# Optimization experiments

Measured on AMD Instinct MI355X. Metric: run time of the kernel, lower is better.

## Reference

```python
import jax, jax.numpy as jnp
import numpy as np

B, T, D, F, H, HID, OUT = 256, 512, 768, 1024, 8, 512, 256
EPS = 1e-5

def setup_inputs() -> dict:
    key = jax.random.key(0)
    ks = jax.random.split(key, 16)
    s = lambda fan_in: 1.0 / np.sqrt(fan_in)
    return {
        "x": jax.random.normal(ks[0], (B, F), jnp.float32),
        "text_feat": jax.random.normal(ks[1], (B, T, D), jnp.float32),
        "attention_mask": jax.random.randint(ks[2], (B, T), 0, 2, jnp.int32),
        # cross-attention params (torch Linear weight layout [out,in])
        "Wq": jax.random.normal(ks[3], (F, F), jnp.float32) * s(F),
        "bq": jnp.zeros((F,), jnp.float32),
        "Wk": jax.random.normal(ks[4], (F, D), jnp.float32) * s(D),
        "bk": jnp.zeros((F,), jnp.float32),
        "Wv": jax.random.normal(ks[5], (F, D), jnp.float32) * s(D),
        "bv": jnp.zeros((F,), jnp.float32),
        "Wo": jax.random.normal(ks[6], (F, F), jnp.float32) * s(F),
        "bo": jnp.zeros((F,), jnp.float32),
        # MLP: hidden Linear -> BatchNorm1d -> GELU, then output Linear
        "W1": jax.random.normal(ks[7], (HID, F), jnp.float32) * s(F),
        "b1": jnp.zeros((HID,), jnp.float32),
        "gamma": jnp.ones((HID,), jnp.float32),
        "beta": jnp.zeros((HID,), jnp.float32),
        "W2": jax.random.normal(ks[8], (OUT, HID), jnp.float32) * s(HID),
        "b2": jnp.zeros((OUT,), jnp.float32),
    }

def _forward(x, text_feat, attention_mask, Wq, bq, Wk, bk, Wv, bv, Wo, bo,
             W1, b1, gamma, beta, W2, b2):
    d = F // H
    q = (x @ Wq.T + bq).reshape(B, H, d)                      # [B,H,d] (q_len=1)
    k = (text_feat @ Wk.T + bk).reshape(B, T, H, d)           # [B,T,H,d]
    v = (text_feat @ Wv.T + bv).reshape(B, T, H, d)
    attn = jnp.einsum('bhd,bthd->bht', q, k) / jnp.sqrt(jnp.float32(d))
    attn = jnp.where(attention_mask[:, None, :] == 0, -jnp.inf, attn)
    attn = jax.nn.softmax(attn, axis=-1)                       # [B,H,T]
    out = jnp.einsum('bht,bthd->bhd', attn, v).reshape(B, F)
    out = out @ Wo.T + bo
    # MLP hidden: linear -> BatchNorm1d (training batch stats) -> GELU (exact)
    h = out @ W1.T + b1
    mu = jnp.mean(h, axis=0)
    var = jnp.var(h, axis=0)
    h = (h - mu) / jnp.sqrt(var + EPS) * gamma + beta
    h = jax.nn.gelu(h, approximate=False)
    return h @ W2.T + b2

def reference(x, text_feat, attention_mask, Wq, bq, Wk, bk, Wv, bv, Wo, bo,
              W1, b1, gamma, beta, W2, b2):
    return _forward(x, text_feat, attention_mask, Wq, bq, Wk, bk, Wv, bv, Wo, bo,
                    W1, b1, gamma, beta, W2, b2)
```

## Files before the change

kernel.cpp:

```cpp
#include <hip/hip_runtime.h>
#include <math.h>

#define Bb   256
#define Tt   512
#define Dd   768
#define Ff   1024
#define Hh   8
#define HIDh 512
#define OUTo 256

__device__ __forceinline__ void tr_tile4(const float* __restrict__ in,
                                         float* __restrict__ out,
                                         int R, int C, int cx, int ry,
                                         float (*tile)[33])
{
    int c0 = cx * 32, r0 = ry * 32;
    int r  = threadIdx.x >> 3;
    int c4 = (threadIdx.x & 7) * 4;
    float4 v = *(const float4*)&in[(size_t)(r0 + r) * C + c0 + c4];
    tile[r][c4 + 0] = v.x;
    tile[r][c4 + 1] = v.y;
    tile[r][c4 + 2] = v.z;
    tile[r][c4 + 3] = v.w;
    __syncthreads();
    float4 o;
    o.x = tile[c4 + 0][r];
    o.y = tile[c4 + 1][r];
    o.z = tile[c4 + 2][r];
    o.w = tile[c4 + 3][r];
    *(float4*)&out[(size_t)(c0 + r) * R + r0 + c4] = o;
}

__global__ __launch_bounds__(256) void prep(const float* __restrict__ Wq, float* __restrict__ WqT,
                                            const float* __restrict__ Wo, float* __restrict__ WoT,
                                            const float* __restrict__ Wv, float* __restrict__ WvT,
                                            const float* __restrict__ W1, float* __restrict__ W1T,
                                            const float* __restrict__ W2, float* __restrict__ W2T,
                                            const float* __restrict__ Wk, float* __restrict__ WkT)
{
    __shared__ float tile[32][33];
    int idx = blockIdx.x;
    if (idx < 1024) {
        tr_tile4(Wq, WqT, 1024, 1024, idx & 31, idx >> 5, tile);
    } else if (idx < 2048) {
        int i2 = idx - 1024;
        tr_tile4(Wo, WoT, 1024, 1024, i2 & 31, i2 >> 5, tile);
    } else if (idx < 2816) {
        int i2 = idx - 2048;
        tr_tile4(Wv, WvT, 1024, 768, i2 % 24, i2 / 24, tile);
    } else if (idx < 3328) {
        int i2 = idx - 2816;
        tr_tile4(W1, W1T, 512, 1024, i2 & 31, i2 >> 5, tile);
    } else if (idx < 3456) {
        int i2 = idx - 3328;
        tr_tile4(W2, W2T, 256, 512, i2 & 15, i2 >> 4, tile);
    } else {
        int i2 = idx - 3456;
        int i = i2 >> 3, h = i2 & 7;
        if (threadIdx.x < 192) {
            int j = threadIdx.x * 4;
            *(float4*)&WkT[(size_t)(i * 8 + h) * 768 + j] =
                *(const float4*)&Wk[(size_t)(h * 128 + i) * 768 + j];
        }
    }
}

#define FMA16(acc, a, w0, w1, w2, w3)                         \
    acc.x = fmaf(a.x, w0.x, acc.x); acc.y = fmaf(a.x, w0.y, acc.y); \
    acc.z = fmaf(a.x, w0.z, acc.z); acc.w = fmaf(a.x, w0.w, acc.w); \
    acc.x = fmaf(a.y, w1.x, acc.x); acc.y = fmaf(a.y, w1.y, acc.y); \
    acc.z = fmaf(a.y, w1.z, acc.z); acc.w = fmaf(a.y, w1.w, acc.w); \
    acc.x = fmaf(a.z, w2.x, acc.x); acc.y = fmaf(a.z, w2.y, acc.y); \
    acc.z = fmaf(a.z, w2.z, acc.z); acc.w = fmaf(a.z, w2.w, acc.w); \
    acc.x = fmaf(a.w, w3.x, acc.x); acc.y = fmaf(a.w, w3.y, acc.y); \
    acc.z = fmaf(a.w, w3.z, acc.z); acc.w = fmaf(a.w, w3.w, acc.w);

template<int CT, int RT, int R, int KS>
__global__ __launch_bounds__(256, 4) void gemm_sk(const float* __restrict__ A, int strideA,
                                                  const float* __restrict__ Wt, int N,
                                                  float* __restrict__ Cslab, int M)
{
    constexpr int CG = CT / 4;
    constexpr int RG = RT / R;
    static_assert(CG * RG == 256, "bad tile");
    const int cg = threadIdx.x % CG;
    const int rg = threadIdx.x / CG;
    const int n0 = blockIdx.x * CT + cg * 4;
    const int r0 = blockIdx.y * RT;
    const int k0 = blockIdx.z * KS;

    __shared__ float As[RT][KS + 4];
    for (int e = threadIdx.x * 4; e < RT * KS; e += 1024) {
        int r = e / KS, k = e % KS;
        *(float4*)&As[r][k] = *(const float4*)&A[(size_t)(r0 + r) * strideA + k0 + k];
    }
    __syncthreads();

    float4 acc[R];
#pragma unroll
    for (int rr = 0; rr < R; ++rr) acc[rr] = make_float4(0.f, 0.f, 0.f, 0.f);
    const float* wp = Wt + (size_t)k0 * N + n0;
#pragma unroll 2
    for (int k = 0; k < KS; k += 4) {
        float4 w0 = *(const float4*)&wp[(size_t)(k + 0) * N];
        float4 w1 = *(const float4*)&wp[(size_t)(k + 1) * N];
        float4 w2 = *(const float4*)&wp[(size_t)(k + 2) * N];
        float4 w3 = *(const float4*)&wp[(size_t)(k + 3) * N];
#pragma unroll
        for (int rr = 0; rr < R; ++rr) {
            float4 a = *(const float4*)&As[rg * R + rr][k];
            FMA16(acc[rr], a, w0, w1, w2, w3)
        }
    }
    float* cp = Cslab + (size_t)blockIdx.z * M * N;
#pragma unroll
    for (int rr = 0; rr < R; ++rr)
        *(float4*)&cp[(size_t)(r0 + rg * R + rr) * N + n0] = acc[rr];
}

template<int S>
__global__ __launch_bounds__(256) void reduce_add(const float* __restrict__ slabs,
                                                  size_t slabstride,
                                                  const float* __restrict__ bias,
                                                  float* __restrict__ out, int N, int total)
{
    int i4 = (blockIdx.x * 256 + threadIdx.x) * 4;
    if (i4 >= total) return;
    float4 acc = *(const float4*)&bias[i4 % N];
#pragma unroll
    for (int s = 0; s < S; ++s) {
        float4 v = *(const float4*)(slabs + (size_t)s * slabstride + i4);
        acc.x += v.x; acc.y += v.y; acc.z += v.z; acc.w += v.w;
    }
    *(float4*)&out[i4] = acc;
}

__global__ __launch_bounds__(256, 4) void qk_gemm(const float* __restrict__ qfull,
                                                  const float* __restrict__ WkT,
                                                  float* __restrict__ qkfull)
{
    const int cg = threadIdx.x & 15;
    const int rg = threadIdx.x >> 4;
    const int cb = blockIdx.x, rb = blockIdx.y;
    const int n0 = cb * 64 + cg * 4;
    const int r0 = rb * 64;
    const int aoff = ((cb * 64) / 768) * 128;

    __shared__ float As[64][132];
    for (int e = threadIdx.x * 4; e < 64 * 128; e += 1024) {
        int r = e >> 7, k = e & 127;
        *(float4*)&As[r][k] = *(const float4*)&qfull[(size_t)(r0 + r) * 1024 + aoff + k];
    }
    __syncthreads();

    float4 acc[4];
#pragma unroll
    for (int rr = 0; rr < 4; ++rr) acc[rr] = make_float4(0.f, 0.f, 0.f, 0.f);
    const float* wp = WkT + n0;
#pragma unroll 2
    for (int k = 0; k < 128; k += 4) {
        float4 w0 = *(const float4*)&wp[(size_t)(k + 0) * 6144];
        float4 w1 = *(const float4*)&wp[(size_t)(k + 1) * 6144];
        float4 w2 = *(const float4*)&wp[(size_t)(k + 2) * 6144];
        float4 w3 = *(const float4*)&wp[(size_t)(k + 3) * 6144];
#pragma unroll
        for (int rr = 0; rr < 4; ++rr) {
            float4 a = *(const float4*)&As[rg * 4 + rr][k];
            FMA16(acc[rr], a, w0, w1, w2, w3)
        }
    }
#pragma unroll
    for (int rr = 0; rr < 4; ++rr)
        *(float4*)&qkfull[(size_t)(r0 + rg * 4 + rr) * 6144 + n0] = acc[rr];
}

__device__ __forceinline__ float dot12(float4 a0, float4 a1, float4 a2,
                                       float4 x0, float4 x1, float4 x2)
{
    float acc;
    acc = a0.x * x0.x;
    acc = fmaf(a0.y, x0.y, acc);
    acc = fmaf(a0.z, x0.z, acc);
    acc = fmaf(a0.w, x0.w, acc);
    acc = fmaf(a1.x, x1.x, acc);
    acc = fmaf(a1.y, x1.y, acc);
    acc = fmaf(a1.z, x1.z, acc);
    acc = fmaf(a1.w, x1.w, acc);
    acc = fmaf(a2.x, x2.x, acc);
    acc = fmaf(a2.y, x2.y, acc);
    acc = fmaf(a2.z, x2.z, acc);
    acc = fmaf(a2.w, x2.w, acc);
    return acc;
}

__global__ __launch_bounds__(256, 2) void attn_part(const float* __restrict__ text,
                                                    const int* __restrict__ mask,
                                                    const float* __restrict__ qk,
                                                    float* __restrict__ pctx,
                                                    float* __restrict__ psum)
{
    const int bx   = blockIdx.x;
    const int b    = bx >> 2;
    const int qt   = bx & 3;
    const int tid  = threadIdx.x;
    const int wv   = tid >> 6;
    const int lane = tid & 63;

    __shared__ float qk_s[Hh][Dd];
    __shared__ float ctx_s[Hh][Dd];
    __shared__ float wsum_s[4][Hh];
    __shared__ int   list_s[128];
    __shared__ int   wcnt_s[2];

    const float* qkp = qk + (size_t)b * (Hh * Dd);
    float* qf = (float*)qk_s;
    float* cf = (float*)ctx_s;
    for (int e = tid * 4; e < Hh * Dd; e += 1024) {
        *(float4*)&qf[e] = *(const float4*)&qkp[e];
        *(float4*)&cf[e] = make_float4(0.f, 0.f, 0.f, 0.f);
    }

    int m = 0, pre = 0, t = 0;
    if (wv < 2) {
        t = qt * 128 + wv * 64 + lane;
        m = mask[(size_t)b * Tt + t];
        unsigned long long bal = __ballot(m != 0);
        pre = __popcll(bal & ((1ull << lane) - 1ull));
        if (lane == 0) wcnt_s[wv] = __popcll(bal);
    }
    __syncthreads();
    if (wv < 2 && m) {
        int base = wv ? wcnt_s[0] : 0;
        list_s[base + pre] = t;
    }
    __syncthreads();
    const int cnt = wcnt_s[0] + wcnt_s[1];

    float s[Hh] = {0.f, 0.f, 0.f, 0.f, 0.f, 0.f, 0.f, 0.f};
    float4 cr[Hh][3];
#pragma unroll
    for (int h = 0; h < Hh; ++h)
#pragma unroll
        for (int c = 0; c < 3; ++c) cr[h][c] = make_float4(0.f, 0.f, 0.f, 0.f);

    const float scale = 0.08838834764831845f;
    const float* tbase = text + (size_t)b * Tt * Dd;

    int e = wv;
    float4 xa0, xa1, xa2, xb0, xb1, xb2;
    xa0 = xa1 = xa2 = make_float4(0.f, 0.f, 0.f, 0.f);
    xb0 = xb1 = xb2 = xa0;
    if (e < cnt) {
        const float* tp = tbase + (size_t)list_s[e] * Dd + 4 * lane;
        xa0 = *(const float4*)(tp);
        xa1 = *(const float4*)(tp + 256);
        xa2 = *(const float4*)(tp + 512);
        int e1 = (e + 4 < cnt) ? e + 4 : cnt - 1;
        const float* tq = tbase + (size_t)list_s[e1] * Dd + 4 * lane;
        xb0 = *(const float4*)(tq);
        xb1 = *(const float4*)(tq + 256);
        xb2 = *(const float4*)(tq + 512);
    }
    while (e < cnt) {
        int ei = (e + 8 < cnt) ? e + 8 : cnt - 1;
        const float* tc = tbase + (size_t)list_s[ei] * Dd + 4 * lane;
        float4 xc0 = *(const float4*)(tc);
        float4 xc1 = *(const float4*)(tc + 256);
        float4 xc2 = *(const float4*)(tc + 512);

        float p[Hh];
#pragma unroll
        for (int h = 0; h < Hh; ++h) {
            const float* qh = &qk_s[h][4 * lane];
            float4 a0 = *(const float4*)(qh);
            float4 a1 = *(const float4*)(qh + 256);
            float4 a2 = *(const float4*)(qh + 512);
            p[h] = dot12(a0, a1, a2, xa0, xa1, xa2);
        }
#pragma unroll
        for (int h = 0; h < Hh; ++h) {
            float v = p[h];
            v += __shfl_xor(v, 1);
            v += __shfl_xor(v, 2);
            v += __shfl_xor(v, 4);
            v += __shfl_xor(v, 8);
            v += __shfl_xor(v, 16);
            v += __shfl_xor(v, 32);
            float w = __expf(v * scale);
            s[h] += w;
            cr[h][0].x = fmaf(w, xa0.x, cr[h][0].x);
            cr[h][0].y = fmaf(w, xa0.y, cr[h][0].y);
            cr[h][0].z = fmaf(w, xa0.z, cr[h][0].z);
            cr[h][0].w = fmaf(w, xa0.w, cr[h][0].w);
            cr[h][1].x = fmaf(w, xa1.x, cr[h][1].x);
            cr[h][1].y = fmaf(w, xa1.y, cr[h][1].y);
            cr[h][1].z = fmaf(w, xa1.z, cr[h][1].z);
            cr[h][1].w = fmaf(w, xa1.w, cr[h][1].w);
            cr[h][2].x = fmaf(w, xa2.x, cr[h][2].x);
            cr[h][2].y = fmaf(w, xa2.y, cr[h][2].y);
            cr[h][2].z = fmaf(w, xa2.z, cr[h][2].z);
            cr[h][2].w = fmaf(w, xa2.w, cr[h][2].w);
        }
        xa0 = xb0; xa1 = xb1; xa2 = xb2;
        xb0 = xc0; xb1 = xc1; xb2 = xc2;
        e += 4;
    }

    if (lane == 0) {
#pragma unroll
        for (int h = 0; h < Hh; ++h) wsum_s[wv][h] = s[h];
    }

    for (int w4 = 0; w4 < 4; ++w4) {
        __syncthreads();
        if (wv == w4) {
#pragma unroll
            for (int h = 0; h < Hh; ++h) {
                float* cp = &ctx_s[h][4 * lane];
#pragma unroll
                for (int c = 0; c < 3; ++c) {
                    float4 cur = *(float4*)(cp + c * 256);
                    cur.x += cr[h][c].x;
                    cur.y += cr[h][c].y;
                    cur.z += cr[h][c].z;
                    cur.w += cr[h][c].w;
                    *(float4*)(cp + c * 256) = cur;
                }
            }
        }
    }
    __syncthreads();

    if (tid < Hh) {
        float S = wsum_s[0][tid] + wsum_s[1][tid] + wsum_s[2][tid] + wsum_s[3][tid];
        psum[(size_t)bx * Hh + tid] = S;
    }
    float* outp = pctx + (size_t)bx * (Hh * Dd);
    for (int e2 = tid * 4; e2 < Hh * Dd; e2 += 1024)
        *(float4*)&outp[e2] = *(const float4*)&cf[e2];
}

__global__ __launch_bounds__(256, 4) void v_gemm(const float* __restrict__ pctx,
                                                 const float* __restrict__ psum,
                                                 const float* __restrict__ WvT,
                                                 float* __restrict__ aoslab)
{
    const int cg = threadIdx.x & 31;
    const int rg = threadIdx.x >> 5;
    const int h = blockIdx.x, rb = blockIdx.y, ks = blockIdx.z;
    const int n0 = h * 128 + cg * 4;
    const int r0 = rb * 32;
    const int k0 = ks * 128;

    __shared__ float As[32][132];
    __shared__ float sv[32];

    if (threadIdx.x < 32) {
        int row = r0 + threadIdx.x;
        float S = 0.f;
#pragma unroll
        for (int i = 0; i < 4; ++i) S += psum[(size_t)(row * 4 + i) * Hh + h];
        sv[threadIdx.x] = 1.0f / S;
    }
    __syncthreads();
    for (int e = threadIdx.x * 4; e < 32 * 128; e += 1024) {
        int r = e >> 7, k = e & 127;
        size_t col = (size_t)h * 768 + k0 + k;
        float4 acc = make_float4(0.f, 0.f, 0.f, 0.f);
#pragma unroll
        for (int i = 0; i < 4; ++i) {
            float4 v = *(const float4*)&pctx[((size_t)(r0 + r) * 4 + i) * 6144 + col];
            acc.x += v.x; acc.y += v.y; acc.z += v.z; acc.w += v.w;
        }
        float svv = sv[r];
        acc.x *= svv; acc.y *= svv; acc.z *= svv; acc.w *= svv;
        *(float4*)&As[r][k] = acc;
    }
    __syncthreads();

    float4 acc[4];
#pragma unroll
    for (int rr = 0; rr < 4; ++rr) acc[rr] = make_float4(0.f, 0.f, 0.f, 0.f);
    const float* wp = WvT + (size_t)k0 * 1024 + n0;
#pragma unroll 2
    for (int k = 0; k < 128; k += 4) {
        float4 w0 = *(const float4*)&wp[(size_t)(k + 0) * 1024];
        float4 w1 = *(const float4*)&wp[(size_t)(k + 1) * 1024];
        float4 w2 = *(const float4*)&wp[(size_t)(k + 2) * 1024];
        float4 w3 = *(const float4*)&wp[(size_t)(k + 3) * 1024];
#pragma unroll
        for (int rr = 0; rr < 4; ++rr) {
            float4 a = *(const float4*)&As[rg * 4 + rr][k];
            FMA16(acc[rr], a, w0, w1, w2, w3)
        }
    }
    float* cp = aoslab + (size_t)ks * 262144;
#pragma unroll
    for (int rr = 0; rr < 4; ++rr)
        *(float4*)&cp[(size_t)(r0 + rg * 4 + rr) * 1024 + n0] = acc[rr];
}

__global__ __launch_bounds__(256) void bn_stats2(const float* __restrict__ h1full,
                                                 const float* __restrict__ gamma,
                                                 const float* __restrict__ beta,
                                                 float* __restrict__ scl,
                                                 float* __restrict__ shf)
{
    int c8 = threadIdx.x & 7, rg = threadIdx.x >> 3;
    int c = blockIdx.x * 8 + c8;
    float sum = 0.f, sq = 0.f;
    for (int r = rg; r < Bb; r += 32) {
        float v = h1full[(size_t)r * HIDh + c];
        sum += v;
        sq = fmaf(v, v, sq);
    }
    __shared__ float ss[32][8], sq_[32][8];
    ss[rg][c8] = sum; sq_[rg][c8] = sq;
    for (int off = 16; off > 0; off >>= 1) {
        __syncthreads();
        if (rg < off) { ss[rg][c8] += ss[rg + off][c8]; sq_[rg][c8] += sq_[rg + off][c8]; }
    }
    __syncthreads();
    if (rg == 0) {
        float mu  = ss[0][c8] * (1.0f / Bb);
        float var = sq_[0][c8] * (1.0f / Bb) - mu * mu;
        float g   = gamma[c] * rsqrtf(var + 1e-5f);
        scl[c] = g;
        shf[c] = fmaf(-mu, g, beta[c]);
    }
}

__global__ __launch_bounds__(256, 4) void gelu2(const float* __restrict__ h1full,
                                                const float* __restrict__ scl,
                                                const float* __restrict__ shf,
                                                const float* __restrict__ W2T,
                                                const float* __restrict__ b2,
                                                float* __restrict__ out)
{
    const int cg = threadIdx.x & 15;
    const int rg = threadIdx.x >> 4;
    const int n0 = blockIdx.x * 64 + cg * 4;
    const int r0 = blockIdx.y * 16;

    __shared__ float As[16][132];
    float4 acc = make_float4(0.f, 0.f, 0.f, 0.f);

    for (int k0 = 0; k0 < HIDh; k0 += 128) {
        __syncthreads();
        for (int e = threadIdx.x * 4; e < 2048; e += 1024) {
            int r = e >> 7, k = e & 127;
            float4 v  = *(const float4*)&h1full[(size_t)(r0 + r) * HIDh + k0 + k];
            float4 sc = *(const float4*)&scl[k0 + k];
            float4 sh = *(const float4*)&shf[k0 + k];
            float4 z;
            z.x = fmaf(v.x, sc.x, sh.x);
            z.y = fmaf(v.y, sc.y, sh.y);
            z.z = fmaf(v.z, sc.z, sh.z);
            z.w = fmaf(v.w, sc.w, sh.w);
            z.x = 0.5f * z.x * (1.0f + erff(z.x * 0.70710678118654752f));
            z.y = 0.5f * z.y * (1.0f + erff(z.y * 0.70710678118654752f));
            z.z = 0.5f * z.z * (1.0f + erff(z.z * 0.70710678118654752f));
            z.w = 0.5f * z.w * (1.0f + erff(z.w * 0.70710678118654752f));
            *(float4*)&As[r][k] = z;
        }
        __syncthreads();
        const float* wp = W2T + (size_t)k0 * OUTo + n0;
#pragma unroll 2
        for (int k = 0; k < 128; k += 4) {
            float4 w0 = *(const float4*)&wp[(size_t)(k + 0) * OUTo];
            float4 w1 = *(const float4*)&wp[(size_t)(k + 1) * OUTo];
            float4 w2 = *(const float4*)&wp[(size_t)(k + 2) * OUTo];
            float4 w3 = *(const float4*)&wp[(size_t)(k + 3) * OUTo];
            float4 a = *(const float4*)&As[rg][k];
            FMA16(acc, a, w0, w1, w2, w3)
        }
    }

    float4 bvv = *(const float4*)&b2[n0];
    acc.x += bvv.x; acc.y += bvv.y; acc.z += bvv.z; acc.w += bvv.w;
    *(float4*)&out[(size_t)(r0 + rg) * OUTo + n0] = acc;
}

extern "C" void kernel_launch(void* const* d_in, const int* in_sizes, int n_in,
                              void* d_out, int out_size, void* d_ws, size_t ws_size,
                              hipStream_t stream)
{
    const float* x     = (const float*)d_in[0];
    const float* text  = (const float*)d_in[1];
    const int*   amask = (const int*)d_in[2];
    const float* Wq    = (const float*)d_in[3];
    const float* bq    = (const float*)d_in[4];
    const float* Wk    = (const float*)d_in[5];
    const float* Wv    = (const float*)d_in[7];
    const float* bv    = (const float*)d_in[8];
    const float* Wo    = (const float*)d_in[9];
    const float* bo    = (const float*)d_in[10];
    const float* W1    = (const float*)d_in[11];
    const float* b1    = (const float*)d_in[12];
    const float* gamma = (const float*)d_in[13];
    const float* beta  = (const float*)d_in[14];
    const float* W2    = (const float*)d_in[15];
    const float* b2    = (const float*)d_in[16];

    float* ws     = (float*)d_ws;
    float* WqT    = ws;
    float* WoT    = WqT    + 1048576;
    float* WkT    = WoT    + 1048576;
    float* WvT    = WkT    + 786432;
    float* W1T    = WvT    + 786432;
    float* W2T    = W1T    + 524288;
    float* qslab  = W2T    + 131072;
    float* qfull  = qslab  + 2097152;
    float* qkfull = qfull  + 262144;
    float* pctx   = qkfull + 1572864;
    float* psum   = pctx   + 6291456;
    float* aoslab = psum   + 8192;
    float* aofull = aoslab + 1572864;
    float* oslab  = aofull + 262144;
    float* ofull  = oslab  + 2097152;
    float* h1slab = ofull  + 262144;
    float* h1full = h1slab + 1048576;
    float* scl    = h1full + 131072;
    float* shf    = scl    + 512;

    prep<<<4480, 256, 0, stream>>>(Wq, WqT, Wo, WoT, Wv, WvT, W1, W1T, W2, W2T, Wk, WkT);

    gemm_sk<64, 64, 4, 128><<<dim3(16, 4, 8), 256, 0, stream>>>(x, 1024, WqT, 1024, qslab, 256);
    reduce_add<8><<<256, 256, 0, stream>>>(qslab, 262144, bq, qfull, 1024, 262144);

    qk_gemm<<<dim3(96, 4), 256, 0, stream>>>(qfull, WkT, qkfull);

    attn_part<<<1024, 256, 0, stream>>>(text, amask, qkfull, pctx, psum);

    v_gemm<<<dim3(8, 8, 6), 256, 0, stream>>>(pctx, psum, WvT, aoslab);
    reduce_add<6><<<256, 256, 0, stream>>>(aoslab, 262144, bv, aofull, 1024, 262144);

    gemm_sk<64, 64, 4, 128><<<dim3(16, 4, 8), 256, 0, stream>>>(aofull, 1024, WoT, 1024, oslab, 256);
    reduce_add<8><<<256, 256, 0, stream>>>(oslab, 262144, bo, ofull, 1024, 262144);

    gemm_sk<64, 64, 4, 128><<<dim3(8, 4, 8), 256, 0, stream>>>(ofull, 1024, W1T, 512, h1slab, 256);
    reduce_add<8><<<128, 256, 0, stream>>>(h1slab, 131072, b1, h1full, 512, 131072);

    bn_stats2<<<64, 256, 0, stream>>>(h1full, gamma, beta, scl, shf);

    gelu2<<<dim3(4, 16), 256, 0, stream>>>(h1full, scl, shf, W2T, b2, (float*)d_out);
}
```

Baseline: 202.9 us.

## Fuse all stages into one cooperative persistent kernel with grid syncs

Replaces the chain of separate kernel launches with a single cooperative persistent kernel of 256 blocks x 512 threads that runs each stage as a phase separated by grid.sync(). GEMM tiles are widened to 128 columns, the attention phase is restructured to a per-batch layout with a smaller ctx buffer in place of pctx/psum partials, and a per-kernel fallback path is kept. The aim is to remove launch gaps and tail effects between the many small stages. In exchange, grid-wide barriers add synchronisation cost and the fixed 256-block grid limits parallelism for the larger phases such as attention.

After: 273.3 us. +34.7%, slower.

```diff
diff --git a/kernel.cpp b/kernel.cpp
--- a/kernel.cpp
+++ b/kernel.cpp
@@ -1,68 +1,65 @@
 #include <hip/hip_runtime.h>
+#include <hip/hip_cooperative_groups.h>
 #include <math.h>
+
+namespace cg = cooperative_groups;
 
 #define Bb   256
 #define Tt   512
 #define Dd   768
-#define Ff   1024
 #define Hh   8
 #define HIDh 512
 #define OUTo 256
 
-__device__ __forceinline__ void tr_tile4(const float* __restrict__ in,
-                                         float* __restrict__ out,
-                                         int R, int C, int cx, int ry,
-                                         float (*tile)[33])
-{
-    int c0 = cx * 32, r0 = ry * 32;
-    int r  = threadIdx.x >> 3;
-    int c4 = (threadIdx.x & 7) * 4;
-    float4 v = *(const float4*)&in[(size_t)(r0 + r) * C + c0 + c4];
-    tile[r][c4 + 0] = v.x;
-    tile[r][c4 + 1] = v.y;
-    tile[r][c4 + 2] = v.z;
-    tile[r][c4 + 3] = v.w;
-    __syncthreads();
-    float4 o;
-    o.x = tile[c4 + 0][r];
-    o.y = tile[c4 + 1][r];
-    o.z = tile[c4 + 2][r];
-    o.w = tile[c4 + 3][r];
-    *(float4*)&out[(size_t)(c0 + r) * R + r0 + c4] = o;
-}
-
-__global__ __launch_bounds__(256) void prep(const float* __restrict__ Wq, float* __restrict__ WqT,
-                                            const float* __restrict__ Wo, float* __restrict__ WoT,
-                                            const float* __restrict__ Wv, float* __restrict__ WvT,
-                                            const float* __restrict__ W1, float* __restrict__ W1T,
-                                            const float* __restrict__ W2, float* __restrict__ W2T,
-                                            const float* __restrict__ Wk, float* __restrict__ WkT)
-{
-    __shared__ float tile[32][33];
-    int idx = blockIdx.x;
-    if (idx < 1024) {
-        tr_tile4(Wq, WqT, 1024, 1024, idx & 31, idx >> 5, tile);
-    } else if (idx < 2048) {
-        int i2 = idx - 1024;
-        tr_tile4(Wo, WoT, 1024, 1024, i2 & 31, i2 >> 5, tile);
-    } else if (idx < 2816) {
-        int i2 = idx - 2048;
-        tr_tile4(Wv, WvT, 1024, 768, i2 % 24, i2 / 24, tile);
-    } else if (idx < 3328) {
-        int i2 = idx - 2816;
-        tr_tile4(W1, W1T, 512, 1024, i2 & 31, i2 >> 5, tile);
-    } else if (idx < 3456) {
-        int i2 = idx - 3328;
-        tr_tile4(W2, W2T, 256, 512, i2 & 15, i2 >> 4, tile);
-    } else {
-        int i2 = idx - 3456;
-        int i = i2 >> 3, h = i2 & 7;
-        if (threadIdx.x < 192) {
-            int j = threadIdx.x * 4;
-            *(float4*)&WkT[(size_t)(i * 8 + h) * 768 + j] =
-                *(const float4*)&Wk[(size_t)(h * 128 + i) * 768 + j];
-        }
-    }
+#define NBLK 256
+#define NTHR 512
+
+union SMem {
+    float tile[2][32][33];
+    struct { float As[64][132]; } g;
+    struct { float qk[Hh][Dd]; float ctx[Hh][Dd];
+             float wsum[Hh][Hh]; float sinv[Hh];
+             int list[Tt]; int wcnt[Hh]; } a;
+    struct { float As[32][132]; } ge;
+    struct { float ss[64][8]; float sq[64][8]; } bn;
+};
+
+struct Params {
+    const float *x, *text;
+    const int   *amask;
+    const float *Wq, *bq, *Wk, *Wv, *bv, *Wo, *bo;
+    const float *W1, *b1, *gamma, *beta, *W2, *b2;
+    float *out, *ws;
+};
+
+struct WS {
+    float *WqT, *WoT, *WkT, *WvT, *W1T, *W2T;
+    float *qslab, *qfull, *qkfull, *ctx;
+    float *aoslab, *aofull, *oslab, *ofull, *h1slab, *h1full, *scl, *shf;
+};
+
+__device__ __host__ inline WS make_ws(float* w)
+{
+    WS s;
+    s.WqT    = w;
+    s.WoT    = s.WqT    + 1048576;
+    s.WkT    = s.WoT    + 1048576;
+    s.WvT    = s.WkT    + 786432;
+    s.W1T    = s.WvT    + 786432;
+    s.W2T    = s.W1T    + 524288;
+    s.qslab  = s.W2T    + 131072;
+    s.qfull  = s.qslab  + 2097152;
+    s.qkfull = s.qfull  + 262144;
+    s.ctx    = s.qkfull + 1572864;
+    s.aoslab = s.ctx    + 1572864;
+    s.aofull = s.aoslab + 1572864;
+    s.oslab  = s.aofull + 262144;
+    s.ofull  = s.oslab  + 2097152;
+    s.h1slab = s.ofull  + 262144;
+    s.h1full = s.h1slab + 1048576;
+    s.scl    = s.h1full + 131072;
+    s.shf    = s.scl    + 512;
+    return s;
 }
 
 #define FMA16(acc, a, w0, w1, w2, w3)                         \
@@ -75,103 +72,145 @@
     acc.x = fmaf(a.w, w3.x, acc.x); acc.y = fmaf(a.w, w3.y, acc.y); \
     acc.z = fmaf(a.w, w3.z, acc.z); acc.w = fmaf(a.w, w3.w, acc.w);
 
-template<int CT, int RT, int R, int KS>
-__global__ __launch_bounds__(256, 4) void gemm_sk(const float* __restrict__ A, int strideA,
-                                                  const float* __restrict__ Wt, int N,
-                                                  float* __restrict__ Cslab, int M)
-{
-    constexpr int CG = CT / 4;
-    constexpr int RG = RT / R;
-    static_assert(CG * RG == 256, "bad tile");
-    const int cg = threadIdx.x % CG;
-    const int rg = threadIdx.x / CG;
-    const int n0 = blockIdx.x * CT + cg * 4;
-    const int r0 = blockIdx.y * RT;
-    const int k0 = blockIdx.z * KS;
-
-    __shared__ float As[RT][KS + 4];
-    for (int e = threadIdx.x * 4; e < RT * KS; e += 1024) {
-        int r = e / KS, k = e % KS;
+__device__ void ph_prep(SMem* sm, const Params& p, const WS& w, int nblk, int bid)
+{
+    const int half = threadIdx.x >> 8;
+    const int tid  = threadIdx.x & 255;
+    for (int base = bid * 2; base < 3456; base += nblk * 2) {
+        int idx = base + half;
+        const float* in; float* out; int R, C, cx, ry;
+        if (idx < 1024)      { in = p.Wq; out = w.WqT; R = 1024; C = 1024; cx = idx & 31; ry = idx >> 5; }
+        else if (idx < 2048) { int i2 = idx - 1024; in = p.Wo; out = w.WoT; R = 1024; C = 1024; cx = i2 & 31; ry = i2 >> 5; }
+        else if (idx < 2816) { int i2 = idx - 2048; in = p.Wv; out = w.WvT; R = 1024; C = 768;  cx = i2 % 24; ry = i2 / 24; }
+        else if (idx < 3328) { int i2 = idx - 2816; in = p.W1; out = w.W1T; R = 512;  C = 1024; cx = i2 & 31; ry = i2 >> 5; }
+        else                 { int i2 = idx - 3328; in = p.W2; out = w.W2T; R = 256;  C = 512;  cx = i2 & 15; ry = i2 >> 4; }
+        float (*tile)[33] = sm->tile[half];
+        int c0 = cx * 32, r0 = ry * 32;
+        int r = tid >> 3, c4 = (tid & 7) * 4;
+        float4 v = *(const float4*)&in[(size_t)(r0 + r) * C + c0 + c4];
+        tile[r][c4 + 0] = v.x;
+        tile[r][c4 + 1] = v.y;
+        tile[r][c4 + 2] = v.z;
+        tile[r][c4 + 3] = v.w;
+        __syncthreads();
+        float4 o;
+        o.x = tile[c4 + 0][r];
+        o.y = tile[c4 + 1][r];
+        o.z = tile[c4 + 2][r];
+        o.w = tile[c4 + 3][r];
+        *(float4*)&out[(size_t)(c0 + r) * R + r0 + c4] = o;
+        __syncthreads();
+    }
+    const float4* src = (const float4*)p.Wk;
+    float4* dst = (float4*)w.WkT;
+    for (int f = bid * NTHR + threadIdx.x; f < 196608; f += nblk * NTHR) {
+        int rem = f / 192, j4 = f % 192;
+        int i = rem >> 3, h = rem & 7;
+        dst[f] = src[(size_t)(h * 128 + i) * 192 + j4];
+    }
+}
+
+__device__ void gemm128x64(SMem* sm, const float* __restrict__ A, int strideA,
+                           const float* __restrict__ Wt, int N,
+                           float* __restrict__ Cslab, int cb, int rb, int ks)
+{
+    float (*As)[132] = sm->g.As;
+    const int cgi = threadIdx.x & 31;
+    const int rg  = threadIdx.x >> 5;
+    const int n0 = cb * 128 + cgi * 4;
+    const int r0 = rb * 64;
+    const int k0 = ks * 128;
+
+    for (int e = threadIdx.x * 4; e < 8192; e += 2048) {
+        int r = e >> 7, k = e & 127;
         *(float4*)&As[r][k] = *(const float4*)&A[(size_t)(r0 + r) * strideA + k0 + k];
     }
     __syncthreads();
 
-    float4 acc[R];
-#pragma unroll
-    for (int rr = 0; rr < R; ++rr) acc[rr] = make_float4(0.f, 0.f, 0.f, 0.f);
+    float4 acc[4];
+#pragma unroll
+    for (int rr = 0; rr < 4; ++rr) acc[rr] = make_float4(0.f, 0.f, 0.f, 0.f);
     const float* wp = Wt + (size_t)k0 * N + n0;
 #pragma unroll 2
-    for (int k = 0; k < KS; k += 4) {
+    for (int k = 0; k < 128; k += 4) {
         float4 w0 = *(const float4*)&wp[(size_t)(k + 0) * N];
         float4 w1 = *(const float4*)&wp[(size_t)(k + 1) * N];
         float4 w2 = *(const float4*)&wp[(size_t)(k + 2) * N];
         float4 w3 = *(const float4*)&wp[(size_t)(k + 3) * N];
 #pragma unroll
-        for (int rr = 0; rr < R; ++rr) {
-            float4 a = *(const float4*)&As[rg * R + rr][k];
-            FMA16(acc[rr], a, w0, w1, w2, w3)
-        }
-    }
-    float* cp = Cslab + (size_t)blockIdx.z * M * N;
-#pragma unroll
-    for (int rr = 0; rr < R; ++rr)
-        *(float4*)&cp[(size_t)(r0 + rg * R + rr) * N + n0] = acc[rr];
-}
-
-template<int S>
-__global__ __launch_bounds__(256) void reduce_add(const float* __restrict__ slabs,
-                                                  size_t slabstride,
-                                                  const float* __restrict__ bias,
-                                                  float* __restrict__ out, int N, int total)
-{
-    int i4 = (blockIdx.x * 256 + threadIdx.x) * 4;
-    if (i4 >= total) return;
-    float4 acc = *(const float4*)&bias[i4 % N];
-#pragma unroll
-    for (int s = 0; s < S; ++s) {
-        float4 v = *(const float4*)(slabs + (size_t)s * slabstride + i4);
-        acc.x += v.x; acc.y += v.y; acc.z += v.z; acc.w += v.w;
-    }
-    *(float4*)&out[i4] = acc;
-}
-
-__global__ __launch_bounds__(256, 4) void qk_gemm(const float* __restrict__ qfull,
-                                                  const float* __restrict__ WkT,
-                                                  float* __restrict__ qkfull)
-{
-    const int cg = threadIdx.x & 15;
-    const int rg = threadIdx.x >> 4;
-    const int cb = blockIdx.x, rb = blockIdx.y;
-    const int n0 = cb * 64 + cg * 4;
-    const int r0 = rb * 64;
-    const int aoff = ((cb * 64) / 768) * 128;
-
-    __shared__ float As[64][132];
-    for (int e = threadIdx.x * 4; e < 64 * 128; e += 1024) {
-        int r = e >> 7, k = e & 127;
-        *(float4*)&As[r][k] = *(const float4*)&qfull[(size_t)(r0 + r) * 1024 + aoff + k];
-    }
-    __syncthreads();
-
-    float4 acc[4];
-#pragma unroll
-    for (int rr = 0; rr < 4; ++rr) acc[rr] = make_float4(0.f, 0.f, 0.f, 0.f);
-    const float* wp = WkT + n0;
-#pragma unroll 2
-    for (int k = 0; k < 128; k += 4) {
-        float4 w0 = *(const float4*)&wp[(size_t)(k + 0) * 6144];
-        float4 w1 = *(const float4*)&wp[(size_t)(k + 1) * 6144];
-        float4 w2 = *(const float4*)&wp[(size_t)(k + 2) * 6144];
-        float4 w3 = *(const float4*)&wp[(size_t)(k + 3) * 6144];
-#pragma unroll
         for (int rr = 0; rr < 4; ++rr) {
             float4 a = *(const float4*)&As[rg * 4 + rr][k];
             FMA16(acc[rr], a, w0, w1, w2, w3)
         }
     }
+    float* cp = Cslab + (size_t)ks * Bb * N;
 #pragma unroll
     for (int rr = 0; rr < 4; ++rr)
-        *(float4*)&qkfull[(size_t)(r0 + rg * 4 + rr) * 6144 + n0] = acc[rr];
+        *(float4*)&cp[(size_t)(r0 + rg * 4 + rr) * N + n0] = acc[rr];
+}
+
+__device__ void ph_qgemm(SMem* sm, const Params& p, const WS& w, int nblk, int bid)
+{
+    for (int j = bid; j < 256; j += nblk) {
+        gemm128x64(sm, p.x, 1024, w.WqT, 1024, w.qslab, j & 7, (j >> 3) & 3, j >> 5);
+        __syncthreads();
+    }
+}
+
+__device__ void ph_ogemm(SMem* sm, const Params& p, const WS& w, int nblk, int bid)
+{
+    for (int j = bid; j < 256; j += nblk) {
+        gemm128x64(sm, w.aofull, 1024, w.WoT, 1024, w.oslab, j & 7, (j >> 3) & 3, j >> 5);
+        __syncthreads();
+    }
+}
+
+__device__ void ph_h1gemm(SMem* sm, const Params& p, const WS& w, int nblk, int bid)
+{
+    for (int j = bid; j < 128; j += nblk) {
+        gemm128x64(sm, w.ofull, 1024, w.W1T, 512, w.h1slab, j & 3, (j >> 2) & 3, j >> 4);
+        __syncthreads();
+    }
+}
+
+__device__ void ph_qk(SMem* sm, const Params& p, const WS& w, int nblk, int bid)
+{
+    for (int j = bid; j < 192; j += nblk) {
+        int cb = j % 48, rb = j / 48;
+        float (*As)[132] = sm->g.As;
+        const int cgi = threadIdx.x & 31;
+        const int rg  = threadIdx.x >> 5;
+        const int n0 = cb * 128 + cgi * 4;
+        const int r0 = rb * 64;
+        const int aoff = (cb / 6) * 128;
+
+        for (int e = threadIdx.x * 4; e < 8192; e += 2048) {
+            int r = e >> 7, k = e & 127;
+            *(float4*)&As[r][k] = *(const float4*)&w.qfull[(size_t)(r0 + r) * 1024 + aoff + k];
+        }
+        __syncthreads();
+
+        float4 acc[4];
+#pragma unroll
+        for (int rr = 0; rr < 4; ++rr) acc[rr] = make_float4(0.f, 0.f, 0.f, 0.f);
+        const float* wp = w.WkT + n0;
+#pragma unroll 2
+        for (int k = 0; k < 128; k += 4) {
+            float4 w0 = *(const float4*)&wp[(size_t)(k + 0) * 6144];
+            float4 w1 = *(const float4*)&wp[(size_t)(k + 1) * 6144];
+            float4 w2 = *(const float4*)&wp[(size_t)(k + 2) * 6144];
+            float4 w3 = *(const float4*)&wp[(size_t)(k + 3) * 6144];
+#pragma unroll
+            for (int rr = 0; rr < 4; ++rr) {
+                float4 a = *(const float4*)&As[rg * 4 + rr][k];
+                FMA16(acc[rr], a, w0, w1, w2, w3)
+            }
+        }
+#pragma unroll
+        for (int rr = 0; rr < 4; ++rr)
+            *(float4*)&w.qkfull[(size_t)(r0 + rg * 4 + rr) * 6144 + n0] = acc[rr];
+        __syncthreads();
+    }
 }
 
 __device__ __forceinline__ float dot12(float4 a0, float4 a1, float4 a2,
@@ -193,355 +232,376 @@
     return acc;
 }
 
-__global__ __launch_bounds__(256, 2) void attn_part(const float* __restrict__ text,
-                                                    const int* __restrict__ mask,
-                                                    const float* __restrict__ qk,
-                                                    float* __restrict__ pctx,
-                                                    float* __restrict__ psum)
-{
-    const int bx   = blockIdx.x;
-    const int b    = bx >> 2;
-    const int qt   = bx & 3;
-    const int tid  = threadIdx.x;
-    const int wv   = tid >> 6;
-    const int lane = tid & 63;
-
-    __shared__ float qk_s[Hh][Dd];
-    __shared__ float ctx_s[Hh][Dd];
-    __shared__ float wsum_s[4][Hh];
-    __shared__ int   list_s[128];
-    __shared__ int   wcnt_s[2];
-
-    const float* qkp = qk + (size_t)b * (Hh * Dd);
-    float* qf = (float*)qk_s;
-    float* cf = (float*)ctx_s;
-    for (int e = tid * 4; e < Hh * Dd; e += 1024) {
-        *(float4*)&qf[e] = *(const float4*)&qkp[e];
-        *(float4*)&cf[e] = make_float4(0.f, 0.f, 0.f, 0.f);
-    }
-
-    int m = 0, pre = 0, t = 0;
-    if (wv < 2) {
-        t = qt * 128 + wv * 64 + lane;
-        m = mask[(size_t)b * Tt + t];
-        unsigned long long bal = __ballot(m != 0);
-        pre = __popcll(bal & ((1ull << lane) - 1ull));
-        if (lane == 0) wcnt_s[wv] = __popcll(bal);
-    }
-    __syncthreads();
-    if (wv < 2 && m) {
-        int base = wv ? wcnt_s[0] : 0;
-        list_s[base + pre] = t;
-    }
-    __syncthreads();
-    const int cnt = wcnt_s[0] + wcnt_s[1];
-
-    float s[Hh] = {0.f, 0.f, 0.f, 0.f, 0.f, 0.f, 0.f, 0.f};
-    float4 cr[Hh][3];
-#pragma unroll
-    for (int h = 0; h < Hh; ++h)
-#pragma unroll
-        for (int c = 0; c < 3; ++c) cr[h][c] = make_float4(0.f, 0.f, 0.f, 0.f);
-
-    const float scale = 0.08838834764831845f;
-    const float* tbase = text + (size_t)b * Tt * Dd;
-
-    int e = wv;
-    float4 xa0, xa1, xa2, xb0, xb1, xb2;
-    xa0 = xa1 = xa2 = make_float4(0.f, 0.f, 0.f, 0.f);
-    xb0 = xb1 = xb2 = xa0;
-    if (e < cnt) {
-        const float* tp = tbase + (size_t)list_s[e] * Dd + 4 * lane;
-        xa0 = *(const float4*)(tp);
-        xa1 = *(const float4*)(tp + 256);
-        xa2 = *(const float4*)(tp + 512);
-        int e1 = (e + 4 < cnt) ? e + 4 : cnt - 1;
-        const float* tq = tbase + (size_t)list_s[e1] * Dd + 4 * lane;
-        xb0 = *(const float4*)(tq);
-        xb1 = *(const float4*)(tq + 256);
-        xb2 = *(const float4*)(tq + 512);
-    }
-    while (e < cnt) {
-        int ei = (e + 8 < cnt) ? e + 8 : cnt - 1;
-        const float* tc = tbase + (size_t)list_s[ei] * Dd + 4 * lane;
-        float4 xc0 = *(const float4*)(tc);
-        float4 xc1 = *(const float4*)(tc + 256);
-        float4 xc2 = *(const float4*)(tc + 512);
-
-        float p[Hh];
-#pragma unroll
-        for (int h = 0; h < Hh; ++h) {
-            const float* qh = &qk_s[h][4 * lane];
-            float4 a0 = *(const float4*)(qh);
-            float4 a1 = *(const float4*)(qh + 256);
-            float4 a2 = *(const float4*)(qh + 512);
-            p[h] = dot12(a0, a1, a2, xa0, xa1, xa2);
-        }
-#pragma unroll
-        for (int h = 0; h < Hh; ++h) {
-            float v = p[h];
-            v += __shfl_xor(v, 1);
-            v += __shfl_xor(v, 2);
-            v += __shfl_xor(v, 4);
-            v += __shfl_xor(v, 8);
-            v += __shfl_xor(v, 16);
-            v += __shfl_xor(v, 32);
-            float w = __expf(v * scale);
-            s[h] += w;
-            cr[h][0].x = fmaf(w, xa0.x, cr[h][0].x);
-            cr[h][0].y = fmaf(w, xa0.y, cr[h][0].y);
-            cr[h][0].z = fmaf(w, xa0.z, cr[h][0].z);
-            cr[h][0].w = fmaf(w, xa0.w, cr[h][0].w);
-            cr[h][1].x = fmaf(w, xa1.x, cr[h][1].x);
-            cr[h][1].y = fmaf(w, xa1.y, cr[h][1].y);
-            cr[h][1].z = fmaf(w, xa1.z, cr[h][1].z);
-            cr[h][1].w = fmaf(w, xa1.w, cr[h][1].w);
-            cr[h][2].x = fmaf(w, xa2.x, cr[h][2].x);
-            cr[h][2].y = fmaf(w, xa2.y, cr[h][2].y);
-            cr[h][2].z = fmaf(w, xa2.z, cr[h][2].z);
-            cr[h][2].w = fmaf(w, xa2.w, cr[h][2].w);
-        }
-        xa0 = xb0; xa1 = xb1; xa2 = xb2;
-        xb0 = xc0; xb1 = xc1; xb2 = xc2;
-        e += 4;
-    }
-
-    if (lane == 0) {
-#pragma unroll
-        for (int h = 0; h < Hh; ++h) wsum_s[wv][h] = s[h];
-    }
-
-    for (int w4 = 0; w4 < 4; ++w4) {
-        __syncthreads();
-        if (wv == w4) {
+__device__ void ph_attn(SMem* sm, const Params& p, const WS& w, int nblk, int bid)
+{
+    for (int b = bid; b < Bb; b += nblk) {
+        const int tid  = threadIdx.x;
+        const int wv   = tid >> 6;
+        const int lane = tid & 63;
+
+        float (*qk_s)[Dd]  = sm->a.qk;
+        float (*ctx_s)[Dd] = sm->a.ctx;
+        float (*wsum_s)[Hh] = sm->a.wsum;
+        int* list_s = sm->a.list;
+        int* wcnt_s = sm->a.wcnt;
+
+        const float* qkp = w.qkfull + (size_t)b * (Hh * Dd);
+        float* qf = (float*)qk_s;
+        float* cf = (float*)ctx_s;
+        for (int e = tid * 4; e < Hh * Dd; e += 2048) {
+            *(float4*)&qf[e] = *(const float4*)&qkp[e];
+            *(float4*)&cf[e] = make_float4(0.f, 0.f, 0.f, 0.f);
+        }
+
+        {
+            int m = p.amask[(size_t)b * Tt + tid];
+            unsigned long long bal = __ballot(m != 0);
+            int pre = __popcll(bal & ((1ull << lane) - 1ull));
+            if (lane == 0) wcnt_s[wv] = __popcll(bal);
+            __syncthreads();
+            if (m) {
+                int base = 0;
+                for (int v = 0; v < wv; ++v) base += wcnt_s[v];
+                list_s[base + pre] = tid;
+            }
+            __syncthreads();
+        }
+        int cnt = 0;
+#pragma unroll
+        for (int v = 0; v < Hh; ++v) cnt += wcnt_s[v];
+
+        float s[Hh] = {0.f, 0.f, 0.f, 0.f, 0.f, 0.f, 0.f, 0.f};
+        float4 cr[Hh][3];
+#pragma unroll
+        for (int h = 0; h < Hh; ++h)
+#pragma unroll
+            for (int c = 0; c < 3; ++c) cr[h][c] = make_float4(0.f, 0.f, 0.f, 0.f);
+
+        const float scale = 0.08838834764831845f;
+        const float* tbase = p.text + (size_t)b * Tt * Dd;
+
+        int e = wv;
+        float4 xa0, xa1, xa2, xb0, xb1, xb2;
+        xa0 = xa1 = xa2 = make_float4(0.f, 0.f, 0.f, 0.f);
+        xb0 = xb1 = xb2 = xa0;
+        if (e < cnt) {
+            const float* tp = tbase + (size_t)list_s[e] * Dd + 4 * lane;
+            xa0 = *(const float4*)(tp);
+            xa1 = *(const float4*)(tp + 256);
+            xa2 = *(const float4*)(tp + 512);
+            int e1 = (e + 8 < cnt) ? e + 8 : cnt - 1;
+            const float* tq = tbase + (size_t)list_s[e1] * Dd + 4 * lane;
+            xb0 = *(const float4*)(tq);
+            xb1 = *(const float4*)(tq + 256);
+            xb2 = *(const float4*)(tq + 512);
+        }
+        while (e < cnt) {
+            int ei = (e + 16 < cnt) ? e + 16 : cnt - 1;
+            const float* tc = tbase + (size_t)list_s[ei] * Dd + 4 * lane;
+            float4 xc0 = *(const float4*)(tc);
+            float4 xc1 = *(const float4*)(tc + 256);
+            float4 xc2 = *(const float4*)(tc + 512);
+
+            float pr[Hh];
 #pragma unroll
             for (int h = 0; h < Hh; ++h) {
-                float* cp = &ctx_s[h][4 * lane];
-#pragma unroll
-                for (int c = 0; c < 3; ++c) {
-                    float4 cur = *(float4*)(cp + c * 256);
-                    cur.x += cr[h][c].x;
-                    cur.y += cr[h][c].y;
-                    cur.z += cr[h][c].z;
-                    cur.w += cr[h][c].w;
-                    *(float4*)(cp + c * 256) = cur;
-                }
-            }
-        }
-    }
-    __syncthreads();
-
-    if (tid < Hh) {
-        float S = wsum_s[0][tid] + wsum_s[1][tid] + wsum_s[2][tid] + wsum_s[3][tid];
-        psum[(size_t)bx * Hh + tid] = S;
-    }
-    float* outp = pctx + (size_t)bx * (Hh * Dd);
-    for (int e2 = tid * 4; e2 < Hh * Dd; e2 += 1024)
-        *(float4*)&outp[e2] = *(const float4*)&cf[e2];
-}
-
-__global__ __launch_bounds__(256, 4) void v_gemm(const float* __restrict__ pctx,
-                                                 const float* __restrict__ psum,
-                                                 const float* __restrict__ WvT,
-                                                 float* __restrict__ aoslab)
-{
-    const int cg = threadIdx.x & 31;
-    const int rg = threadIdx.x >> 5;
-    const int h = blockIdx.x, rb = blockIdx.y, ks = blockIdx.z;
-    const int n0 = h * 128 + cg * 4;
-    const int r0 = rb * 32;
-    const int k0 = ks * 128;
-
-    __shared__ float As[32][132];
-    __shared__ float sv[32];
-
-    if (threadIdx.x < 32) {
-        int row = r0 + threadIdx.x;
-        float S = 0.f;
-#pragma unroll
-        for (int i = 0; i < 4; ++i) S += psum[(size_t)(row * 4 + i) * Hh + h];
-        sv[threadIdx.x] = 1.0f / S;
-    }
-    __syncthreads();
-    for (int e = threadIdx.x * 4; e < 32 * 128; e += 1024) {
-        int r = e >> 7, k = e & 127;
-        size_t col = (size_t)h * 768 + k0 + k;
-        float4 acc = make_float4(0.f, 0.f, 0.f, 0.f);
-#pragma unroll
-        for (int i = 0; i < 4; ++i) {
-            float4 v = *(const float4*)&pctx[((size_t)(r0 + r) * 4 + i) * 6144 + col];
-            acc.x += v.x; acc.y += v.y; acc.z += v.z; acc.w += v.w;
-        }
-        float svv = sv[r];
-        acc.x *= svv; acc.y *= svv; acc.z *= svv; acc.w *= svv;
-        *(float4*)&As[r][k] = acc;
-    }
-    __syncthreads();
-
-    float4 acc[4];
-#pragma unroll
-    for (int rr = 0; rr < 4; ++rr) acc[rr] = make_float4(0.f, 0.f, 0.f, 0.f);
-    const float* wp = WvT + (size_t)k0 * 1024 + n0;
-#pragma unroll 2
-    for (int k = 0; k < 128; k += 4) {
-        float4 w0 = *(const float4*)&wp[(size_t)(k + 0) * 1024];
-        float4 w1 = *(const float4*)&wp[(size_t)(k + 1) * 1024];
-        float4 w2 = *(const float4*)&wp[(size_t)(k + 2) * 1024];
-        float4 w3 = *(const float4*)&wp[(size_t)(k + 3) * 1024];
-#pragma unroll
-        for (int rr = 0; rr < 4; ++rr) {
-            float4 a = *(const float4*)&As[rg * 4 + rr][k];
-            FMA16(acc[rr], a, w0, w1, w2, w3)
-        }
-    }
-    float* cp = aoslab + (size_t)ks * 262144;
-#pragma unroll
-    for (int rr = 0; rr < 4; ++rr)
-        *(float4*)&cp[(size_t)(r0 + rg * 4 + rr) * 1024 + n0] = acc[rr];
-}
-
-__global__ __launch_bounds__(256) void bn_stats2(const float* __restrict__ h1full,
-                                                 const float* __restrict__ gamma,
-                                                 const float* __restrict__ beta,
-                                                 float* __restrict__ scl,
-                                                 float* __restrict__ shf)
-{
-    int c8 = threadIdx.x & 7, rg = threadIdx.x >> 3;
-    int c = blockIdx.x * 8 + c8;
-    float sum = 0.f, sq = 0.f;
-    for (int r = rg; r < Bb; r += 32) {
-        float v = h1full[(size_t)r * HIDh + c];
-        sum += v;
-        sq = fmaf(v, v, sq);
-    }
-    __shared__ float ss[32][8], sq_[32][8];
-    ss[rg][c8] = sum; sq_[rg][c8] = sq;
-    for (int off = 16; off > 0; off >>= 1) {
-        __syncthreads();
-        if (rg < off) { ss[rg][c8] += ss[rg + off][c8]; sq_[rg][c8] += sq_[rg + off][c8]; }
-    }
-    __syncthreads();
-    if (rg == 0) {
-        float mu  = ss[0][c8] * (1.0f / Bb);
-        float var = sq_[0][c8] * (1.0f / Bb) - mu * mu;
-        float g   = gamma[c] * rsqrtf(var + 1e-5f);
-        scl[c] = g;
-        shf[c] = fmaf(-mu, g, beta[c]);
-    }
-}
-
-__global__ __launch_bounds__(256, 4) void gelu2(const float* __restrict__ h1full,
-                                                const float* __restrict__ scl,
-                                                const float* __restrict__ shf,
-                                                const float* __restrict__ W2T,
-                                                const float* __restrict__ b2,
-                                                float* __restrict__ out)
-{
-    const int cg = threadIdx.x & 15;
-    const int rg = threadIdx.x >> 4;
-    const int n0 = blockIdx.x * 64 + cg * 4;
-    const int r0 = blockIdx.y * 16;
-
-    __shared__ float As[16][132];
-    float4 acc = make_float4(0.f, 0.f, 0.f, 0.f);
-
-    for (int k0 = 0; k0 < HIDh; k0 += 128) {
-        __syncthreads();
-        for (int e = threadIdx.x * 4; e < 2048; e += 1024) {
+                const float* qh = &qk_s[h][4 * lane];
+                float4 a0 = *(const float4*)(qh);
+                float4 a1 = *(const float4*)(qh + 256);
+                float4 a2 = *(const float4*)(qh + 512);
+                pr[h] = dot12(a0, a1, a2, xa0, xa1, xa2);
+            }
+#pragma unroll
+            for (int h = 0; h < Hh; ++h) {
+                float v = pr[h];
+                v += __shfl_xor(v, 1);
+                v += __shfl_xor(v, 2);
+                v += __shfl_xor(v, 4);
+                v += __shfl_xor(v, 8);
+                v += __shfl_xor(v, 16);
+                v += __shfl_xor(v, 32);
+                float wt = __expf(v * scale);
+                s[h] += wt;
+                cr[h][0].x = fmaf(wt, xa0.x, cr[h][0].x);
+                cr[h][0].y = fmaf(wt, xa0.y, cr[h][0].y);
+                cr[h][0].z = fmaf(wt, xa0.z, cr[h][0].z);
+                cr[h][0].w = fmaf(wt, xa0.w, cr[h][0].w);
+                cr[h][1].x = fmaf(wt, xa1.x, cr[h][1].x);
+                cr[h][1].y = fmaf(wt, xa1.y, cr[h][1].y);
+                cr[h][1].z = fmaf(wt, xa1.z, cr[h][1].z);
+                cr[h][1].w = fmaf(wt, xa1.w, cr[h][1].w);
+                cr[h][2].x = fmaf(wt, xa2.x, cr[h][2].x);
+                cr[h][2].y = fmaf(wt, xa2.y, cr[h][2].y);
+                cr[h][2].z = fmaf(wt, xa2.z, cr[h][2].z);
+                cr[h][2].w = fmaf(wt, xa2.w, cr[h][2].w);
+            }
+            xa0 = xb0; xa1 = xb1; xa2 = xb2;
+            xb0 = xc0; xb1 = xc1; xb2 = xc2;
+            e += 8;
+        }
+
+        if (lane == 0) {
+#pragma unroll
+            for (int h = 0; h < Hh; ++h) wsum_s[wv][h] = s[h];
+        }
+
+        for (int rnd = 0; rnd < 8; ++rnd) {
+            __syncthreads();
+            int h = (wv + rnd) & 7;
+            float* cp = &ctx_s[h][4 * lane];
+#pragma unroll
+            for (int c = 0; c < 3; ++c) {
+                float4 cu = *(float4*)(cp + c * 256);
+                cu.x += cr[h][c].x;
+                cu.y += cr[h][c].y;
+                cu.z += cr[h][c].z;
+                cu.w += cr[h][c].w;
+                *(float4*)(cp + c * 256) = cu;
+            }
+        }
+        __syncthreads();
+
+        if (tid < Hh) {
+            float S = 0.f;
+#pragma unroll
+            for (int v = 0; v < Hh; ++v) S += wsum_s[v][tid];
+            sm->a.sinv[tid] = 1.0f / S;
+        }
+        __syncthreads();
+
+        float* outp = w.ctx + (size_t)b * (Hh * Dd);
+        for (int e2 = tid * 4; e2 < Hh * Dd; e2 += 2048) {
+            float4 v = *(const float4*)&cf[e2];
+            float si = sm->a.sinv[e2 / Dd];
+            v.x *= si; v.y *= si; v.z *= si; v.w *= si;
+            *(float4*)&outp[e2] = v;
+        }
+        __syncthreads();
+    }
+}
+
+__device__ void ph_v(SMem* sm, const Params& p, const WS& w, int nblk, int bid)
+{
+    for (int j = bid; j < 192; j += nblk) {
+        int h = j & 7, rb = (j >> 3) & 3, ks = j >> 5;
+        float (*As)[132] = sm->g.As;
+        const int cgi = threadIdx.x & 31;
+        const int rg  = threadIdx.x >> 5;
+        const int n0 = h * 128 + cgi * 4;
+        const int r0 = rb * 64;
+        const int k0 = ks * 128;
+
+        for (int e = threadIdx.x * 4; e < 8192; e += 2048) {
             int r = e >> 7, k = e & 127;
-            float4 v  = *(const float4*)&h1full[(size_t)(r0 + r) * HIDh + k0 + k];
-            float4 sc = *(const float4*)&scl[k0 + k];
-            float4 sh = *(const float4*)&shf[k0 + k];
-            float4 z;
-            z.x = fmaf(v.x, sc.x, sh.x);
-            z.y = fmaf(v.y, sc.y, sh.y);
-            z.z = fmaf(v.z, sc.z, sh.z);
-            z.w = fmaf(v.w, sc.w, sh.w);
-            z.x = 0.5f * z.x * (1.0f + erff(z.x * 0.70710678118654752f));
-            z.y = 0.5f * z.y * (1.0f + erff(z.y * 0.70710678118654752f));
-            z.z = 0.5f * z.z * (1.0f + erff(z.z * 0.70710678118654752f));
-            z.w = 0.5f * z.w * (1.0f + erff(z.w * 0.70710678118654752f));
-            *(float4*)&As[r][k] = z;
-        }
-        __syncthreads();
-        const float* wp = W2T + (size_t)k0 * OUTo + n0;
+            *(float4*)&As[r][k] =
+                *(const float4*)&w.ctx[(size_t)(r0 + r) * 6144 + (size_t)h * 768 + k0 + k];
+        }
+        __syncthreads();
+
+        float4 acc[4];
+#pragma unroll
+        for (int rr = 0; rr < 4; ++rr) acc[rr] = make_float4(0.f, 0.f, 0.f, 0.f);
+        const float* wp = w.WvT + (size_t)k0 * 1024 + n0;
 #pragma unroll 2
         for (int k = 0; k < 128; k += 4) {
-            float4 w0 = *(const float4*)&wp[(size_t)(k + 0) * OUTo];
-            float4 w1 = *(const float4*)&wp[(size_t)(k + 1) * OUTo];
-            float4 w2 = *(const float4*)&wp[(size_t)(k + 2) * OUTo];
-            float4 w3 = *(const float4*)&wp[(size_t)(k + 3) * OUTo];
-            float4 a = *(const float4*)&As[rg][k];
-            FMA16(acc, a, w0, w1, w2, w3)
-        }
-    }
-
-    float4 bvv = *(const float4*)&b2[n0];
-    acc.x += bvv.x; acc.y += bvv.y; acc.z += bvv.z; acc.w += bvv.w;
-    *(float4*)&out[(size_t)(r0 + rg) * OUTo + n0] = acc;
-}
+            float4 w0 = *(const float4*)&wp[(size_t)(k + 0) * 1024];
+            float4 w1 = *(const float4*)&wp[(size_t)(k + 1) * 1024];
+            float4 w2 = *(const float4*)&wp[(size_t)(k + 2) * 1024];
+            float4 w3 = *(const float4*)&wp[(size_t)(k + 3) * 1024];
+#pragma unroll
+            for (int rr = 0; rr < 4; ++rr) {
+                float4 a = *(const float4*)&As[rg * 4 + rr][k];
+                FMA16(acc[rr], a, w0, w1, w2, w3)
+            }
+        }
+        float* cp = w.aoslab + (size_t)ks * 262144;
+#pragma unroll
+        for (int rr = 0; rr < 4; ++rr)
+            *(float4*)&cp[(size_t)(r0 + rg * 4 + rr) * 1024 + n0] = acc[rr];
+        __syncthreads();
+    }
+}
+
+__device__ void reduce_phase(const float* __restrict__ slabs, int S, size_t slabstride,
+                             const float* __restrict__ bias, float* __restrict__ outp,
+                             int N, int total, int nblk, int bid)
+{
+    for (int i4 = (bid * NTHR + threadIdx.x) * 4; i4 < total; i4 += nblk * NTHR * 4) {
+        float4 acc = *(const float4*)&bias[i4 % N];
+        for (int s = 0; s < S; ++s) {
+            float4 v = *(const float4*)(slabs + (size_t)s * slabstride + i4);
+            acc.x += v.x; acc.y += v.y; acc.z += v.z; acc.w += v.w;
+        }
+        *(float4*)&outp[i4] = acc;
+    }
+}
+
+__device__ void ph_bn(SMem* sm, const Params& p, const WS& w, int nblk, int bid)
+{
+    for (int j = bid; j < 64; j += nblk) {
+        int c8 = threadIdx.x & 7, rg = threadIdx.x >> 3;
+        int c = j * 8 + c8;
+        float sum = 0.f, sq = 0.f;
+        for (int r = rg; r < Bb; r += 64) {
+            float v = w.h1full[(size_t)r * HIDh + c];
+            sum += v;
+            sq = fmaf(v, v, sq);
+        }
+        float (*ss)[8] = sm->bn.ss;
+        float (*sq_)[8] = sm->bn.sq;
+        ss[rg][c8] = sum; sq_[rg][c8] = sq;
+        for (int off = 32; off > 0; off >>= 1) {
+            __syncthreads();
+            if (rg < off) { ss[rg][c8] += ss[rg + off][c8]; sq_[rg][c8] += sq_[rg + off][c8]; }
+        }
+        __syncthreads();
+        if (rg == 0) {
+            float mu  = ss[0][c8] * (1.0f / Bb);
+            float var = sq_[0][c8] * (1.0f / Bb) - mu * mu;
+            float g   = p.gamma[c] * rsqrtf(var + 1e-5f);
+            w.scl[c] = g;
+            w.shf[c] = fmaf(-mu, g, p.beta[c]);
+        }
+        __syncthreads();
+    }
+}
+
+__device__ void ph_gelu(SMem* sm, const Params& p, const WS& w, int nblk, int bid)
+{
+    for (int j = bid; j < 32; j += nblk) {
+        int cb = j & 3, rb = j >> 2;
+        float (*As)[132] = sm->ge.As;
+        const int cgi = threadIdx.x & 15;
+        const int rg  = threadIdx.x >> 4;
+        const int n0 = cb * 64 + cgi * 4;
+        const int r0 = rb * 32;
+
+        float4 acc = make_float4(0.f, 0.f, 0.f, 0.f);
+        for (int k0 = 0; k0 < HIDh; k0 += 128) {
+            __syncthreads();
+            for (int e = threadIdx.x * 4; e < 4096; e += 2048) {
+                int r = e >> 7, k = e & 127;
+                float4 v  = *(const float4*)&w.h1full[(size_t)(r0 + r) * HIDh + k0 + k];
+                float4 sc = *(const float4*)&w.scl[k0 + k];
+                float4 sh = *(const float4*)&w.shf[k0 + k];
+                float4 z;
+                z.x = fmaf(v.x, sc.x, sh.x);
+                z.y = fmaf(v.y, sc.y, sh.y);
+                z.z = fmaf(v.z, sc.z, sh.z);
+                z.w = fmaf(v.w, sc.w, sh.w);
+                z.x = 0.5f * z.x * (1.0f + erff(z.x * 0.70710678118654752f));
+                z.y = 0.5f * z.y * (1.0f + erff(z.y * 0.70710678118654752f));
+                z.z = 0.5f * z.z * (1.0f + erff(z.z * 0.70710678118654752f));
+                z.w = 0.5f * z.w * (1.0f + erff(z.w * 0.70710678118654752f));
+                *(float4*)&As[r][k] = z;
+            }
+            __syncthreads();
+            const float* wp = w.W2T + (size_t)k0 * OUTo + n0;
+#pragma unroll 2
+            for (int k = 0; k < 128; k += 4) {
+                float4 w0 = *(const float4*)&wp[(size_t)(k + 0) * OUTo];
+                float4 w1 = *(const float4*)&wp[(size_t)(k + 1) * OUTo];
+                float4 w2 = *(const float4*)&wp[(size_t)(k + 2) * OUTo];
+                float4 w3 = *(const float4*)&wp[(size_t)(k + 3) * OUTo];
+                float4 a = *(const float4*)&As[rg][k];
+                FMA16(acc, a, w0, w1, w2, w3)
+            }
+        }
+        float4 bvv = *(const float4*)&p.b2[n0];
+        acc.x += bvv.x; acc.y += bvv.y; acc.z += bvv.z; acc.w += bvv.w;
+        *(float4*)&p.out[(size_t)(r0 + rg) * OUTo + n0] = acc;
+        __syncthreads();
+    }
+}
+
+__global__ __launch_bounds__(NTHR, 2) void mega(Params p)
+{
+    __shared__ SMem sm;
+    WS w = make_ws(p.ws);
+    cg::grid_group grid = cg::this_grid();
+
+    ph_prep(&sm, p, w, NBLK, blockIdx.x);                                     grid.sync();
+    ph_qgemm(&sm, p, w, NBLK, blockIdx.x);                                    grid.sync();
+    reduce_phase(w.qslab, 8, 262144, p.bq, w.qfull, 1024, 262144, NBLK, blockIdx.x);  grid.sync();
+    ph_qk(&sm, p, w, NBLK, blockIdx.x);                                       grid.sync();
+    ph_attn(&sm, p, w, NBLK, blockIdx.x);                                     grid.sync();
+    ph_v(&sm, p, w, NBLK, blockIdx.x);                                        grid.sync();
+    reduce_phase(w.aoslab, 6, 262144, p.bv, w.aofull, 1024, 262144, NBLK, blockIdx.x); grid.sync();
+    ph_ogemm(&sm, p, w, NBLK, blockIdx.x);                                    grid.sync();
+    reduce_phase(w.oslab, 8, 262144, p.bo, w.ofull, 1024, 262144, NBLK, blockIdx.x);   grid.sync();
+    ph_h1gemm(&sm, p, w, NBLK, blockIdx.x);                                   grid.sync();
+    reduce_phase(w.h1slab, 8, 131072, p.b1, w.h1full, 512, 131072, NBLK, blockIdx.x);  grid.sync();
+    ph_bn(&sm, p, w, NBLK, blockIdx.x);                                       grid.sync();
+    ph_gelu(&sm, p, w, NBLK, blockIdx.x);
+}
+
+#define FBK(name, body)                                                     \
+__global__ __launch_bounds__(NTHR, 2) void name(Params p) {                 \
+    __shared__ SMem sm; WS w = make_ws(p.ws); (void)w; (void)sm;            \
+    body;                                                                   \
+}
+FBK(k_prep,   ph_prep(&sm, p, w, gridDim.x, blockIdx.x))
+FBK(k_qgemm,  ph_qgemm(&sm, p, w, gridDim.x, blockIdx.x))
+FBK(k_redq,   reduce_phase(w.qslab, 8, 262144, p.bq, w.qfull, 1024, 262144, gridDim.x, blockIdx.x))
+FBK(k_qk,     ph_qk(&sm, p, w, gridDim.x, blockIdx.x))
+FBK(k_attn,   ph_attn(&sm, p, w, gridDim.x, blockIdx.x))
+FBK(k_v,      ph_v(&sm, p, w, gridDim.x, blockIdx.x))
+FBK(k_redao,  reduce_phase(w.aoslab, 6, 262144, p.bv, w.aofull, 1024, 262144, gridDim.x, blockIdx.x))
+FBK(k_ogemm,  ph_ogemm(&sm, p, w, gridDim.x, blockIdx.x))
+FBK(k_redo,   reduce_phase(w.oslab, 8, 262144, p.bo, w.ofull, 1024, 262144, gridDim.x, blockIdx.x))
+FBK(k_h1gemm, ph_h1gemm(&sm, p, w, gridDim.x, blockIdx.x))
+FBK(k_redh1,  reduce_phase(w.h1slab, 8, 131072, p.b1, w.h1full, 512, 131072, gridDim.x, blockIdx.x))
+FBK(k_bn,     ph_bn(&sm, p, w, gridDim.x, blockIdx.x))
+FBK(k_gelu,   ph_gelu(&sm, p, w, gridDim.x, blockIdx.x))
 
 extern "C" void kernel_launch(void* const* d_in, const int* in_sizes, int n_in,
                               void* d_out, int out_size, void* d_ws, size_t ws_size,
                               hipStream_t stream)
 {
-    const float* x     = (const float*)d_in[0];
-    const float* text  = (const float*)d_in[1];
-    const int*   amask = (const int*)d_in[2];
-    const float* Wq    = (const float*)d_in[3];
-    const float* bq    = (const float*)d_in[4];
-    const float* Wk    = (const float*)d_in[5];
-    const float* Wv    = (const float*)d_in[7];
-    const float* bv    = (const float*)d_in[8];
-    const float* Wo    = (const float*)d_in[9];
-    const float* bo    = (const float*)d_in[10];
-    const float* W1    = (const float*)d_in[11];
-    const float* b1    = (const float*)d_in[12];
-    const float* gamma = (const float*)d_in[13];
-    const float* beta  = (const float*)d_in[14];
-    const float* W2    = (const float*)d_in[15];
-    const float* b2    = (const float*)d_in[16];
-
-    float* ws     = (float*)d_ws;
-    float* WqT    = ws;
-    float* WoT    = WqT    + 1048576;
-    float* WkT    = WoT    + 1048576;
-    float* WvT    = WkT    + 786432;
-    float* W1T    = WvT    + 786432;
-    float* W2T    = W1T    + 524288;
-    float* qslab  = W2T    + 131072;
-    float* qfull  = qslab  + 2097152;
-    float* qkfull = qfull  + 262144;
-    float* pctx   = qkfull + 1572864;
-    float* psum   = pctx   + 6291456;
-    float* aoslab = psum   + 8192;
-    float* aofull = aoslab + 1572864;
-    float* oslab  = aofull + 262144;
-    float* ofull  = oslab  + 2097152;
-    float* h1slab = ofull  + 262144;
-    float* h1full = h1slab + 1048576;
-    float* scl    = h1full + 131072;
-    float* shf    = scl    + 512;
-
-    prep<<<4480, 256, 0, stream>>>(Wq, WqT, Wo, WoT, Wv, WvT, W1, W1T, W2, W2T, Wk, WkT);
-
-    gemm_sk<64, 64, 4, 128><<<dim3(16, 4, 8), 256, 0, stream>>>(x, 1024, WqT, 1024, qslab, 256);
-    reduce_add<8><<<256, 256, 0, stream>>>(qslab, 262144, bq, qfull, 1024, 262144);
-
-    qk_gemm<<<dim3(96, 4), 256, 0, stream>>>(qfull, WkT, qkfull);
-
-    attn_part<<<1024, 256, 0, stream>>>(text, amask, qkfull, pctx, psum);
-
-    v_gemm<<<dim3(8, 8, 6), 256, 0, stream>>>(pctx, psum, WvT, aoslab);
-    reduce_add<6><<<256, 256, 0, stream>>>(aoslab, 262144, bv, aofull, 1024, 262144);
-
-    gemm_sk<64, 64, 4, 128><<<dim3(16, 4, 8), 256, 0, stream>>>(aofull, 1024, WoT, 1024, oslab, 256);
-    reduce_add<8><<<256, 256, 0, stream>>>(oslab, 262144, bo, ofull, 1024, 262144);
-
-    gemm_sk<64, 64, 4, 128><<<dim3(8, 4, 8), 256, 0, stream>>>(ofull, 1024, W1T, 512, h1slab, 256);
-    reduce_add<8><<<128, 256, 0, stream>>>(h1slab, 131072, b1, h1full, 512, 131072);
-
-    bn_stats2<<<64, 256, 0, stream>>>(h1full, gamma, beta, scl, shf);
-
-    gelu2<<<dim3(4, 16), 256, 0, stream>>>(h1full, scl, shf, W2T, b2, (float*)d_out);
-}
+    Params p;
+    p.x     = (const float*)d_in[0];
+    p.text  = (const float*)d_in[1];
+    p.amask = (const int*)d_in[2];
+    p.Wq    = (const float*)d_in[3];
+    p.bq    = (const float*)d_in[4];
+    p.Wk    = (const float*)d_in[5];
+    p.Wv    = (const float*)d_in[7];
+    p.bv    = (const float*)d_in[8];
+    p.Wo    = (const float*)d_in[9];
+    p.bo    = (const float*)d_in[10];
+    p.W1    = (const float*)d_in[11];
+    p.b1    = (const float*)d_in[12];
+    p.gamma = (const float*)d_in[13];
+    p.beta  = (const float*)d_in[14];
+    p.W2    = (const float*)d_in[15];
+    p.b2    = (const float*)d_in[16];
+    p.out   = (float*)d_out;
+    p.ws    = (float*)d_ws;
+
+    int dev = 0;
+    hipGetDevice(&dev);
+    int coop = 0, ncu = 0, maxb = 0;
+    hipDeviceGetAttribute(&coop, hipDeviceAttributeCooperativeLaunch, dev);
+    hipDeviceGetAttribute(&ncu, hipDeviceAttributeMultiprocessorCount, dev);
+    hipOccupancyMaxActiveBlocksPerMultiprocessor(&maxb, reinterpret_cast<const void*>(mega), NTHR, 0);
+
+    if (coop && (long)maxb * ncu >= NBLK) {
+        void* args[] = { (void*)&p };
+        hipLaunchCooperativeKernel(reinterpret_cast<void*>(mega),
+                                   dim3(NBLK), dim3(NTHR), args, 0, stream);
+    } else {
+        k_prep  <<<NBLK, NTHR, 0, stream>>>(p);
+        k_qgemm <<<NBLK, NTHR, 0, stream>>>(p);
+        k_redq  <<<128,  NTHR, 0, stream>>>(p);
+        k_qk    <<<192,  NTHR, 0, stream>>>(p);
+        k_attn  <<<NBLK, NTHR, 0, stream>>>(p);
+        k_v     <<<192,  NTHR, 0, stream>>>(p);
+        k_redao <<<128,  NTHR, 0, stream>>>(p);
+        k_ogemm <<<NBLK, NTHR, 0, stream>>>(p);
+        k_redo  <<<128,  NTHR, 0, stream>>>(p);
+        k_h1gemm<<<128,  NTHR, 0, stream>>>(p);
+        k_redh1 <<<64,   NTHR, 0, stream>>>(p);
+        k_bn    <<<64,   NTHR, 0, stream>>>(p);
+        k_gelu  <<<32,   NTHR, 0, stream>>>(p);
+    }
+}
```
